# Kernel tuning notes

Hardware: AMD Instinct MI355X
Metric: run time of the kernel (lower is better)

The kernel has to match this reference:

```python
import jax, jax.numpy as jnp
import numpy as np


def setup_inputs() -> dict:
    key = jax.random.key(0)
    ks = jax.random.split(key, 7)
    G, MC, B = 4, 100, 512
    IN, H, OUT = 456, 400, 10
    return {
        "x": jax.random.normal(ks[0], (B, IN), dtype=jnp.float32),
        "mu1": jax.random.normal(ks[1], (G, IN, H), dtype=jnp.float32),
        "sigma1": jax.random.normal(ks[2], (G, IN, H), dtype=jnp.float32),
        "mu3": jax.random.normal(ks[3], (G, H, OUT), dtype=jnp.float32),
        "sigma3": jax.random.normal(ks[4], (G, H, OUT), dtype=jnp.float32),
        "zeta1": jax.random.normal(ks[5], (G, MC, B, H), dtype=jnp.float32),
        "zeta3": jax.random.normal(ks[6], (G, MC, B, OUT), dtype=jnp.float32),
        "num": 3,
    }


def reference(x, mu1, sigma1, mu3, sigma3, zeta1, zeta3, num):
    # softplus(sigma)^2, the local-reparameterization variance term
    sp2 = lambda s: jnp.square(jnp.log1p(jnp.exp(s)))

    def one_net(m1, s1, m3, s3, z1, z3):
        # layer 1: local reparameterization trick (Kingma et al. 2015)
        g1 = x @ m1                               # [B, H]
        d1 = (x * x) @ sp2(s1)                    # [B, H]
        h = jax.nn.relu(g1 + jnp.sqrt(d1) * z1)   # [MC, B, H] via broadcast
        # layer 2
        g3 = jnp.einsum('mbh,ho->mbo', h, m3)     # [MC, B, OUT]
        d3 = jnp.einsum('mbh,ho->mbo', h * h, sp2(s3))
        o = jax.nn.relu(g3 + jnp.sqrt(d3) * z3)
        p = jax.nn.softmax(o, axis=-1)            # nn.Softmax over class dim
        return p.mean(axis=0)                     # average over MC samples

    G = num + 1
    outs = jax.vmap(one_net)(mu1[:G], sigma1[:G], mu3[:G], sigma3[:G],
                             zeta1[:G], zeta3[:G])  # [G, B, OUT]
    B = x.shape[0]
    # torch.cat((out_0, out_1, ...), dim=1)
    return jnp.transpose(outs, (1, 0, 2)).reshape(B, -1)
```

## Files before the change

kernel.cpp:

```cpp
#include <hip/hip_runtime.h>
#include <math.h>

#define GN  4
#define MCN 100
#define BN  512
#define INN 456
#define HN  400
#define ON  10

__device__ __forceinline__ float sp2f(float s) {
    float l = log1pf(__expf(-fabsf(s)));
    float r = fmaxf(s, 0.0f) + l;
    return r * r;
}

#define DPP_ADD(v, CTRL) \
    ((v) + __int_as_float(__builtin_amdgcn_update_dpp( \
        0, __float_as_int(v), (CTRL), 0xF, 0xF, true)))

__device__ __forceinline__ float reduce16(float v) {
    v = DPP_ADD(v, 0xB1);
    v = DPP_ADD(v, 0x4E);
    v = DPP_ADD(v, 0x124);
    v = DPP_ADD(v, 0x128);
    return v;
}

__global__ __launch_bounds__(256) void k_transpose(
    const float* __restrict__ x, float* __restrict__ xT, float* __restrict__ xxT) {
    __shared__ float tile[64][65];
    int it = blockIdx.x;
    int bt = blockIdx.y;
    int tx = threadIdx.x & 63;
    int ty = threadIdx.x >> 6;
    int i_in = it * 64 + tx;
    #pragma unroll
    for (int r = 0; r < 16; ++r) {
        int row = r * 4 + ty;
        int b = bt * 64 + row;
        tile[row][tx] = (i_in < INN) ? x[b * INN + i_in] : 0.0f;
    }
    __syncthreads();
    #pragma unroll
    for (int r = 0; r < 16; ++r) {
        int row = r * 4 + ty;
        int i = it * 64 + row;
        if (i < INN) {
            float v = tile[tx][row];
            xT[i * BN + bt * 64 + tx]  = v;
            xxT[i * BN + bt * 64 + tx] = v * v;
        }
    }
}

__global__ __launch_bounds__(256) void k_sp(
    const float* __restrict__ sigma1, const float* __restrict__ sigma3,
    float* __restrict__ sp1, float* __restrict__ sp3) {
    int idx = blockIdx.x * 256 + threadIdx.x;
    const int n1 = GN * INN * HN / 4;
    const int n3 = GN * HN * ON / 4;
    if (idx < n1) {
        float4 s = ((const float4*)sigma1)[idx];
        float4 o;
        o.x = sp2f(s.x); o.y = sp2f(s.y); o.z = sp2f(s.z); o.w = sp2f(s.w);
        ((float4*)sp1)[idx] = o;
    } else if (idx < n1 + n3) {
        int k = idx - n1;
        float4 s = ((const float4*)sigma3)[k];
        float4 o;
        o.x = sp2f(s.x); o.y = sp2f(s.y); o.z = sp2f(s.z); o.w = sp2f(s.w);
        ((float4*)sp3)[k] = o;
    }
}

__global__ __launch_bounds__(256) void k_layer1(
    const float* __restrict__ xT, const float* __restrict__ xxT,
    const float* __restrict__ mu1, const float* __restrict__ sp1,
    float* __restrict__ A, float* __restrict__ S) {
    int bt = blockIdx.x;
    int ht = blockIdx.y;
    int g  = blockIdx.z;
    int lane = threadIdx.x & 63;
    int wv   = threadIdx.x >> 6;
    int h = ht * 64 + lane;
    bool hv = h < HN;
    int hc = hv ? h : (HN - 1);
    int b0 = __builtin_amdgcn_readfirstlane(bt * 16 + wv * 4);
    const float* mp = mu1 + (size_t)g * INN * HN + hc;
    const float* pp = sp1 + (size_t)g * INN * HN + hc;
    float accA[4] = {0.f, 0.f, 0.f, 0.f};
    float accD[4] = {0.f, 0.f, 0.f, 0.f};
    #pragma unroll 4
    for (int k = 0; k < INN; ++k) {
        float a = mp[(size_t)k * HN];
        float p = pp[(size_t)k * HN];
        float4 xv  = *(const float4*)(xT  + k * BN + b0);
        float4 xxv = *(const float4*)(xxT + k * BN + b0);
        accA[0] = fmaf(a, xv.x,  accA[0]);
        accA[1] = fmaf(a, xv.y,  accA[1]);
        accA[2] = fmaf(a, xv.z,  accA[2]);
        accA[3] = fmaf(a, xv.w,  accA[3]);
        accD[0] = fmaf(p, xxv.x, accD[0]);
        accD[1] = fmaf(p, xxv.y, accD[1]);
        accD[2] = fmaf(p, xxv.z, accD[2]);
        accD[3] = fmaf(p, xxv.w, accD[3]);
    }
    if (hv) {
        #pragma unroll
        for (int j = 0; j < 4; ++j) {
            size_t o = ((size_t)g * BN + (b0 + j)) * HN + h;
            A[o] = accA[j];
            S[o] = sqrtf(accD[j]);
        }
    }
}

template<int NI>
__device__ __forceinline__ void mc_chunk(
    int g, int b, int mb, int kc, int og, int rgg, int t,
    const float* __restrict__ zeta1, const float* __restrict__ zeta3,
    const float* as_s, const float* wp, float* epi, float* psum) {
    const int NR = NI * 8;

    float acc[NI][ON];
    #pragma unroll
    for (int i = 0; i < NI; ++i)
        #pragma unroll
        for (int o = 0; o < ON; ++o) acc[i][o] = 0.0f;

    const float* zp[NI];
    #pragma unroll
    for (int i = 0; i < NI; ++i) {
        int m = mb + rgg + 8 * i;
        int mcl = m < MCN ? m : (MCN - 1);
        zp[i] = zeta1 + ((size_t)(g * MCN + mcl) * BN + b) * HN + 4 * kc;
    }

    float4 zc[NI];
    #pragma unroll
    for (int i = 0; i < NI; ++i) zc[i] = *(const float4*)(zp[i]);

    #pragma unroll 1
    for (int j = 0; j < 6; ++j) {
        float4 zn[NI];
        if (j < 5) {
            #pragma unroll
            for (int i = 0; i < NI; ++i) zn[i] = *(const float4*)(zp[i] + 64 * (j + 1));
        } else {
            #pragma unroll
            for (int i = 0; i < NI; ++i) zn[i] = zc[i];
        }
        int k0 = 4 * kc + 64 * j;
        float4 as01 = *(const float4*)(as_s + 2 * k0);
        float4 as23 = *(const float4*)(as_s + 2 * k0 + 4);
        float4 W[ON];
        #pragma unroll
        for (int o = 0; o < ON; ++o) W[o] = *(const float4*)(wp + o * HN + k0);
        #pragma unroll
        for (int i = 0; i < NI; ++i) {
            float h0 = fmaxf(0.0f, fmaf(as01.y, zc[i].x, as01.x));
            float h1 = fmaxf(0.0f, fmaf(as01.w, zc[i].y, as01.z));
            float h2 = fmaxf(0.0f, fmaf(as23.y, zc[i].z, as23.x));
            float h3 = fmaxf(0.0f, fmaf(as23.w, zc[i].w, as23.z));
            float c0 = og ? h0 * h0 : h0;
            float c1 = og ? h1 * h1 : h1;
            float c2 = og ? h2 * h2 : h2;
            float c3 = og ? h3 * h3 : h3;
            #pragma unroll
            for (int o = 0; o < ON; ++o) {
                acc[i][o] = fmaf(c0, W[o].x, acc[i][o]);
                acc[i][o] = fmaf(c1, W[o].y, acc[i][o]);
                acc[i][o] = fmaf(c2, W[o].z, acc[i][o]);
                acc[i][o] = fmaf(c3, W[o].w, acc[i][o]);
            }
        }
        #pragma unroll
        for (int i = 0; i < NI; ++i) zc[i] = zn[i];
    }

    {
        int k = 384 + kc;
        int toff = 384 - 3 * kc;
        float2 as = *(const float2*)(as_s + 2 * k);
        float wt[ON];
        #pragma unroll
        for (int o = 0; o < ON; ++o) wt[o] = wp[o * HN + k];
        #pragma unroll
        for (int i = 0; i < NI; ++i) {
            float z = zp[i][toff];
            float hv = fmaxf(0.0f, fmaf(as.y, z, as.x));
            float c = og ? hv * hv : hv;
            #pragma unroll
            for (int o = 0; o < ON; ++o) acc[i][o] = fmaf(c, wt[o], acc[i][o]);
        }
    }

    #pragma unroll
    for (int i = 0; i < NI; ++i)
        #pragma unroll
        for (int o = 0; o < ON; ++o) acc[i][o] = reduce16(acc[i][o]);

    if (kc == 0) {
        #pragma unroll
        for (int i = 0; i < NI; ++i) {
            int rl = rgg + 8 * i;
            #pragma unroll
            for (int o = 0; o < ON; ++o)
                epi[(rl * ON + o) * 2 + og] = acc[i][o];
        }
    }
    __syncthreads();

    if (t < NR) {
        int m = mb + t;
        if (m < MCN) {
            const float* z3p = zeta3 + ((size_t)(g * MCN + m) * BN + b) * ON;
            float ov[ON];
            float mx = 0.0f;
            #pragma unroll
            for (int o = 0; o < ON; ++o) {
                float2 gd = *(const float2*)(epi + (t * ON + o) * 2);
                float v = fmaf(sqrtf(gd.y), z3p[o], gd.x);
                v = fmaxf(v, 0.0f);
                ov[o] = v;
                mx = fmaxf(mx, v);
            }
            float se = 0.0f;
            #pragma unroll
            for (int o = 0; o < ON; ++o) { float e = __expf(ov[o] - mx); ov[o] = e; se += e; }
            float r = 1.0f / se;
            #pragma unroll
            for (int o = 0; o < ON; ++o) psum[o] = fmaf(ov[o], r, psum[o]);
        }
    }
    __syncthreads();
}

__global__ __launch_bounds__(256, 3) void k_layer2(
    const float* __restrict__ A, const float* __restrict__ S,
    const float* __restrict__ mu3, const float* __restrict__ sp3,
    const float* __restrict__ zeta1, const float* __restrict__ zeta3,
    float* __restrict__ out) {
    int b = blockIdx.x;
    int g = blockIdx.y;

    __shared__ __align__(16) float wT_s[ON * HN];
    __shared__ __align__(16) float vT_s[ON * HN];
    __shared__ __align__(16) float as_s[2 * HN];
    __shared__ __align__(16) float epi[32 * ON * 2];
    __shared__ __align__(16) float psh[32 * ON];

    int t = threadIdx.x;

    {
        const float* wsrc = mu3 + (size_t)g * HN * ON;
        const float* vsrc = sp3 + (size_t)g * HN * ON;
        for (int i = t; i < HN * ON; i += 256) {
            int h = i / ON, o = i - h * ON;
            wT_s[o * HN + h] = wsrc[i];
            vT_s[o * HN + h] = vsrc[i];
        }
    }
    for (int i = t; i < HN; i += 256) {
        size_t src = ((size_t)g * BN + b) * HN + i;
        as_s[2 * i]     = A[src];
        as_s[2 * i + 1] = S[src];
    }
    __syncthreads();

    int kc  = t & 15;
    int og  = (t >> 4) & 1;
    int rgg = t >> 5;

    const float* wp = og ? vT_s : wT_s;

    float psum[ON];
    #pragma unroll
    for (int o = 0; o < ON; ++o) psum[o] = 0.0f;

    #pragma unroll 1
    for (int c = 0; c < 3; ++c)
        mc_chunk<4>(g, b, c * 32, kc, og, rgg, t, zeta1, zeta3, as_s, wp, epi, psum);
    mc_chunk<1>(g, b, 96, kc, og, rgg, t, zeta1, zeta3, as_s, wp, epi, psum);

    if (t < 32) {
        #pragma unroll
        for (int o = 0; o < ON; ++o) psh[t * ON + o] = psum[o];
    }
    __syncthreads();
    if (t < ON) {
        float s = 0.0f;
        #pragma unroll
        for (int r = 0; r < 32; ++r) s += psh[r * ON + t];
        out[b * (GN * ON) + g * ON + t] = s * (1.0f / MCN);
    }
}

extern "C" void kernel_launch(void* const* d_in, const int* in_sizes, int n_in,
                              void* d_out, int out_size, void* d_ws, size_t ws_size,
                              hipStream_t stream) {
    const float* x      = (const float*)d_in[0];
    const float* mu1    = (const float*)d_in[1];
    const float* sigma1 = (const float*)d_in[2];
    const float* mu3    = (const float*)d_in[3];
    const float* sigma3 = (const float*)d_in[4];
    const float* zeta1  = (const float*)d_in[5];
    const float* zeta3  = (const float*)d_in[6];

    float* ws  = (float*)d_ws;
    float* xT  = ws;
    float* xxT = xT  + INN * BN;
    float* sp1 = xxT + INN * BN;
    float* sp3 = sp1 + GN * INN * HN;
    float* A   = sp3 + GN * HN * ON;
    float* S   = A   + GN * BN * HN;
    float* out = (float*)d_out;

    const int nsp = GN * INN * HN / 4 + GN * HN * ON / 4;
    k_transpose<<<dim3(8, 8), 256, 0, stream>>>(x, xT, xxT);
    k_sp<<<dim3((nsp + 255) / 256), 256, 0, stream>>>(sigma1, sigma3, sp1, sp3);
    k_layer1<<<dim3(32, 7, GN), 256, 0, stream>>>(xT, xxT, mu1, sp1, A, S);
    k_layer2<<<dim3(BN, GN), 256, 0, stream>>>(A, S, mu3, sp3, zeta1, zeta3, out);
}
```

Baseline: 565.9 us.

## Re-split layer-2 reduction lanes, pad hidden dim, use nontemporal zeta loads

Reorganises the layer-2 MC kernel. Each output group now spans 32 hidden-dim lanes instead of 16, and covers 4 MC rows instead of 8, so the 100 MC samples are processed as 6×16 plus 4 rows with no clamped duplicate rows. The hidden dimension is padded to 416 with zeroed weights, and A and S move into separate shared arrays. zeta1 and zeta3 are read with nontemporal loads, zeta3 is prefetched before the reduction, and block indices are swizzled across batch and group. These changes aim to cut redundant work and cache pollution from the streamed zeta tensors. In exchange they add an extra half-sum in the epilogue and more chunk iterations with more __syncthreads.

```diff
diff --git a/kernel.cpp b/kernel.cpp
--- a/kernel.cpp
+++ b/kernel.cpp
@@ -7,11 +7,22 @@
 #define INN 456
 #define HN  400
 #define ON  10
+#define HP  416
 
 __device__ __forceinline__ float sp2f(float s) {
     float l = log1pf(__expf(-fabsf(s)));
     float r = fmaxf(s, 0.0f) + l;
     return r * r;
+}
+
+typedef float f4v __attribute__((ext_vector_type(4)));
+typedef float f2v __attribute__((ext_vector_type(2)));
+
+__device__ __forceinline__ f4v nt4(const float* p) {
+    return __builtin_nontemporal_load((const f4v*)p);
+}
+__device__ __forceinline__ float nt1(const float* p) {
+    return __builtin_nontemporal_load(p);
 }
 
 #define DPP_ADD(v, CTRL) \
@@ -119,8 +130,16 @@
 __device__ __forceinline__ void mc_chunk(
     int g, int b, int mb, int kc, int og, int rgg, int t,
     const float* __restrict__ zeta1, const float* __restrict__ zeta3,
-    const float* as_s, const float* wp, float* epi, float* psum) {
-    const int NR = NI * 8;
+    const float* a_s, const float* s_s, const float* wp,
+    float* epi, float* psum) {
+    const int NR = NI * 4;
+
+    float z3r[ON];
+    if (t < NR) {
+        const float* z3p = zeta3 + ((size_t)(g * MCN + mb + t) * BN + b) * ON;
+        #pragma unroll
+        for (int o = 0; o < ON; ++o) z3r[o] = nt1(z3p + o);
+    }
 
     float acc[NI][ON];
     #pragma unroll
@@ -131,47 +150,46 @@
     const float* zp[NI];
     #pragma unroll
     for (int i = 0; i < NI; ++i) {
-        int m = mb + rgg + 8 * i;
-        int mcl = m < MCN ? m : (MCN - 1);
-        zp[i] = zeta1 + ((size_t)(g * MCN + mcl) * BN + b) * HN + 4 * kc;
-    }
-
-    float4 zc[NI];
-    #pragma unroll
-    for (int i = 0; i < NI; ++i) zc[i] = *(const float4*)(zp[i]);
+        int m = mb + rgg + 4 * i;
+        zp[i] = zeta1 + ((size_t)(g * MCN + m) * BN + b) * HN + 4 * kc;
+    }
+
+    f4v zc[NI];
+    #pragma unroll
+    for (int i = 0; i < NI; ++i) zc[i] = nt4(zp[i]);
 
     #pragma unroll 1
-    for (int j = 0; j < 6; ++j) {
-        float4 zn[NI];
-        if (j < 5) {
-            #pragma unroll
-            for (int i = 0; i < NI; ++i) zn[i] = *(const float4*)(zp[i] + 64 * (j + 1));
+    for (int j = 0; j < 3; ++j) {
+        f4v zn[NI];
+        if (j < 2) {
+            #pragma unroll
+            for (int i = 0; i < NI; ++i) zn[i] = nt4(zp[i] + 128 * (j + 1));
         } else {
             #pragma unroll
             for (int i = 0; i < NI; ++i) zn[i] = zc[i];
         }
-        int k0 = 4 * kc + 64 * j;
-        float4 as01 = *(const float4*)(as_s + 2 * k0);
-        float4 as23 = *(const float4*)(as_s + 2 * k0 + 4);
-        float4 W[ON];
-        #pragma unroll
-        for (int o = 0; o < ON; ++o) W[o] = *(const float4*)(wp + o * HN + k0);
+        int k0 = 4 * kc + 128 * j;
+        f4v Av = *(const f4v*)(a_s + k0);
+        f4v Sv = *(const f4v*)(s_s + k0);
+        f4v W[ON];
+        #pragma unroll
+        for (int o = 0; o < ON; ++o) W[o] = *(const f4v*)(wp + o * HP + k0);
         #pragma unroll
         for (int i = 0; i < NI; ++i) {
-            float h0 = fmaxf(0.0f, fmaf(as01.y, zc[i].x, as01.x));
-            float h1 = fmaxf(0.0f, fmaf(as01.w, zc[i].y, as01.z));
-            float h2 = fmaxf(0.0f, fmaf(as23.y, zc[i].z, as23.x));
-            float h3 = fmaxf(0.0f, fmaf(as23.w, zc[i].w, as23.z));
+            float h0 = fmaxf(0.0f, fmaf(Sv[0], zc[i][0], Av[0]));
+            float h1 = fmaxf(0.0f, fmaf(Sv[1], zc[i][1], Av[1]));
+            float h2 = fmaxf(0.0f, fmaf(Sv[2], zc[i][2], Av[2]));
+            float h3 = fmaxf(0.0f, fmaf(Sv[3], zc[i][3], Av[3]));
             float c0 = og ? h0 * h0 : h0;
             float c1 = og ? h1 * h1 : h1;
             float c2 = og ? h2 * h2 : h2;
             float c3 = og ? h3 * h3 : h3;
             #pragma unroll
             for (int o = 0; o < ON; ++o) {
-                acc[i][o] = fmaf(c0, W[o].x, acc[i][o]);
-                acc[i][o] = fmaf(c1, W[o].y, acc[i][o]);
-                acc[i][o] = fmaf(c2, W[o].z, acc[i][o]);
-                acc[i][o] = fmaf(c3, W[o].w, acc[i][o]);
+                acc[i][o] = fmaf(c0, W[o][0], acc[i][o]);
+                acc[i][o] = fmaf(c1, W[o][1], acc[i][o]);
+                acc[i][o] = fmaf(c2, W[o][2], acc[i][o]);
+                acc[i][o] = fmaf(c3, W[o][3], acc[i][o]);
             }
         }
         #pragma unroll
@@ -179,17 +197,19 @@
     }
 
     {
-        int k = 384 + kc;
-        int toff = 384 - 3 * kc;
-        float2 as = *(const float2*)(as_s + 2 * k);
+        int k_as = 384 + kc;
+        int k_z  = (kc < 16) ? (384 + kc) : 399;
+        int dz   = k_z - 4 * kc;
+        float Aa = a_s[k_as];
+        float Ss = s_s[k_as];
         float wt[ON];
         #pragma unroll
-        for (int o = 0; o < ON; ++o) wt[o] = wp[o * HN + k];
+        for (int o = 0; o < ON; ++o) wt[o] = wp[o * HP + k_as];
         #pragma unroll
         for (int i = 0; i < NI; ++i) {
-            float z = zp[i][toff];
-            float hv = fmaxf(0.0f, fmaf(as.y, z, as.x));
-            float c = og ? hv * hv : hv;
+            float z  = nt1(zp[i] + dz);
+            float hv = fmaxf(0.0f, fmaf(Ss, z, Aa));
+            float c  = og ? hv * hv : hv;
             #pragma unroll
             for (int o = 0; o < ON; ++o) acc[i][o] = fmaf(c, wt[o], acc[i][o]);
         }
@@ -200,38 +220,37 @@
         #pragma unroll
         for (int o = 0; o < ON; ++o) acc[i][o] = reduce16(acc[i][o]);
 
-    if (kc == 0) {
+    if ((kc & 15) == 0) {
+        int half = kc >> 4;
         #pragma unroll
         for (int i = 0; i < NI; ++i) {
-            int rl = rgg + 8 * i;
+            int rl = rgg + 4 * i;
             #pragma unroll
             for (int o = 0; o < ON; ++o)
-                epi[(rl * ON + o) * 2 + og] = acc[i][o];
+                epi[(rl * ON + o) * 4 + og * 2 + half] = acc[i][o];
         }
     }
     __syncthreads();
 
     if (t < NR) {
-        int m = mb + t;
-        if (m < MCN) {
-            const float* z3p = zeta3 + ((size_t)(g * MCN + m) * BN + b) * ON;
-            float ov[ON];
-            float mx = 0.0f;
-            #pragma unroll
-            for (int o = 0; o < ON; ++o) {
-                float2 gd = *(const float2*)(epi + (t * ON + o) * 2);
-                float v = fmaf(sqrtf(gd.y), z3p[o], gd.x);
-                v = fmaxf(v, 0.0f);
-                ov[o] = v;
-                mx = fmaxf(mx, v);
-            }
-            float se = 0.0f;
-            #pragma unroll
-            for (int o = 0; o < ON; ++o) { float e = __expf(ov[o] - mx); ov[o] = e; se += e; }
-            float r = 1.0f / se;
-            #pragma unroll
-            for (int o = 0; o < ON; ++o) psum[o] = fmaf(ov[o], r, psum[o]);
-        }
+        float ov[ON];
+        float mx = 0.0f;
+        #pragma unroll
+        for (int o = 0; o < ON; ++o) {
+            const float* e = epi + (t * ON + o) * 4;
+            float gg = e[0] + e[1];
+            float gd = e[2] + e[3];
+            float v = fmaf(sqrtf(gd), z3r[o], gg);
+            v = fmaxf(v, 0.0f);
+            ov[o] = v;
+            mx = fmaxf(mx, v);
+        }
+        float se = 0.0f;
+        #pragma unroll
+        for (int o = 0; o < ON; ++o) { float e = __expf(ov[o] - mx); ov[o] = e; se += e; }
+        float r = 1.0f / se;
+        #pragma unroll
+        for (int o = 0; o < ON; ++o) psum[o] = fmaf(ov[o], r, psum[o]);
     }
     __syncthreads();
 }
@@ -241,14 +260,17 @@
     const float* __restrict__ mu3, const float* __restrict__ sp3,
     const float* __restrict__ zeta1, const float* __restrict__ zeta3,
     float* __restrict__ out) {
-    int b = blockIdx.x;
-    int g = blockIdx.y;
-
-    __shared__ __align__(16) float wT_s[ON * HN];
-    __shared__ __align__(16) float vT_s[ON * HN];
-    __shared__ __align__(16) float as_s[2 * HN];
-    __shared__ __align__(16) float epi[32 * ON * 2];
-    __shared__ __align__(16) float psh[32 * ON];
+    int lin = blockIdx.x + BN * blockIdx.y;
+    int nid = (lin & 7) * (BN * GN / 8) + (lin >> 3);
+    int b = nid & (BN - 1);
+    int g = nid >> 9;
+
+    __shared__ __align__(16) float wT_s[ON * HP];
+    __shared__ __align__(16) float vT_s[ON * HP];
+    __shared__ __align__(16) float a_s[HP];
+    __shared__ __align__(16) float s_s[HP];
+    __shared__ __align__(16) float epi[16 * ON * 4];
+    __shared__ __align__(16) float psh[16 * ON];
 
     int t = threadIdx.x;
 
@@ -257,20 +279,30 @@
         const float* vsrc = sp3 + (size_t)g * HN * ON;
         for (int i = t; i < HN * ON; i += 256) {
             int h = i / ON, o = i - h * ON;
-            wT_s[o * HN + h] = wsrc[i];
-            vT_s[o * HN + h] = vsrc[i];
-        }
-    }
-    for (int i = t; i < HN; i += 256) {
-        size_t src = ((size_t)g * BN + b) * HN + i;
-        as_s[2 * i]     = A[src];
-        as_s[2 * i + 1] = S[src];
-    }
-    __syncthreads();
-
-    int kc  = t & 15;
-    int og  = (t >> 4) & 1;
-    int rgg = t >> 5;
+            wT_s[o * HP + h] = wsrc[i];
+            vT_s[o * HP + h] = vsrc[i];
+        }
+        for (int i = t; i < (HP - HN) * ON; i += 256) {
+            int o = i / (HP - HN), h = HN + i % (HP - HN);
+            wT_s[o * HP + h] = 0.0f;
+            vT_s[o * HP + h] = 0.0f;
+        }
+    }
+    for (int i = t; i < HP; i += 256) {
+        if (i < HN) {
+            size_t src = ((size_t)g * BN + b) * HN + i;
+            a_s[i] = A[src];
+            s_s[i] = S[src];
+        } else {
+            a_s[i] = 0.0f;
+            s_s[i] = 0.0f;
+        }
+    }
+    __syncthreads();
+
+    int kc  = t & 31;
+    int og  = (t >> 5) & 1;
+    int rgg = t >> 6;
 
     const float* wp = og ? vT_s : wT_s;
 
@@ -279,11 +311,11 @@
     for (int o = 0; o < ON; ++o) psum[o] = 0.0f;
 
     #pragma unroll 1
-    for (int c = 0; c < 3; ++c)
-        mc_chunk<4>(g, b, c * 32, kc, og, rgg, t, zeta1, zeta3, as_s, wp, epi, psum);
-    mc_chunk<1>(g, b, 96, kc, og, rgg, t, zeta1, zeta3, as_s, wp, epi, psum);
-
-    if (t < 32) {
+    for (int c = 0; c < 6; ++c)
+        mc_chunk<4>(g, b, c * 16, kc, og, rgg, t, zeta1, zeta3, a_s, s_s, wp, epi, psum);
+    mc_chunk<1>(g, b, 96, kc, og, rgg, t, zeta1, zeta3, a_s, s_s, wp, epi, psum);
+
+    if (t < 16) {
         #pragma unroll
         for (int o = 0; o < ON; ++o) psh[t * ON + o] = psum[o];
     }
@@ -291,7 +323,7 @@
     if (t < ON) {
         float s = 0.0f;
         #pragma unroll
-        for (int r = 0; r < 32; ++r) s += psh[r * ON + t];
+        for (int r = 0; r < 16; ++r) s += psh[r * ON + t];
         out[b * (GN * ON) + g * ON + t] = s * (1.0f / MCN);
     }
 }
```

New measurement: 737.8 us. 30.4% more time.
